# Kernel optimization log

Hardware: AMD Instinct MI355X
Metric: run time of the kernel (lower is better)

## Reference

```python
import jax, jax.numpy as jnp
import numpy as np
import math

VOCAB = 50257
BLOCK = 2048
NE = 768


def setup_inputs() -> dict:
    key = jax.random.key(0)
    ks = jax.random.split(key, 12)
    s = 0.02
    idx = jax.random.randint(ks[0], (4, 2048), 0, VOCAB, dtype=jnp.int64 if jax.config.jax_enable_x64 else jnp.int32)
    tok_emb = jax.random.normal(ks[1], (VOCAB, NE), jnp.float32) * s
    pos_emb = jax.random.normal(ks[2], (BLOCK, NE), jnp.float32) * s
    Wk = jax.random.normal(ks[3], (NE, NE), jnp.float32) * s
    bk = jnp.zeros((NE,), jnp.float32)
    Wq = jax.random.normal(ks[4], (NE, NE), jnp.float32) * s
    bq = jnp.zeros((NE,), jnp.float32)
    Wv = jax.random.normal(ks[5], (NE, NE), jnp.float32) * s
    bv = jnp.zeros((NE,), jnp.float32)
    ln_g = jnp.ones((NE,), jnp.float32)
    ln_b = jnp.zeros((NE,), jnp.float32)
    Wh = jax.random.normal(ks[6], (NE, VOCAB), jnp.float32) * s
    bh = jnp.zeros((VOCAB,), jnp.float32)
    return {"idx": idx, "tok_emb": tok_emb, "pos_emb": pos_emb, "Wq": Wq, "bq": bq,
            "Wk": Wk, "bk": bk, "Wv": Wv, "bv": bv, "ln_g": ln_g, "ln_b": ln_b,
            "Wh": Wh, "bh": bh}


def reference(idx, tok_emb, pos_emb, Wq, bq, Wk, bk, Wv, bv, ln_g, ln_b, Wh, bh):
    B, T = idx.shape
    C = tok_emb.shape[1]
    x = tok_emb[idx] + pos_emb[:T]  # [B,T,C]
    q = jnp.einsum('btc,cd->btd', x, Wq) + bq
    k = jnp.einsum('btc,cd->btd', x, Wk) + bk
    v = jnp.einsum('btc,cd->btd', x, Wv) + bv
    att = jnp.einsum('btd,bsd->bts', q, k) / math.sqrt(C)  # [B,T,T]
    causal = jnp.tril(jnp.ones((T, T), bool))
    att = jnp.where(causal, att, -jnp.inf)
    att = jax.nn.softmax(att, axis=-1)
    y = jnp.einsum('bts,bsd->btd', att, v)
    # LayerNorm (eps=1e-5, torch default)
    mu = jnp.mean(y, axis=-1, keepdims=True)
    var = jnp.mean((y - mu) ** 2, axis=-1, keepdims=True)
    yn = (y - mu) * jax.lax.rsqrt(var + 1e-5) * ln_g + ln_b
    logits = jnp.einsum('btc,cv->btv', yn, Wh) + bh
    return logits
```

## Files before the change

kernel.cpp:

```cpp
#include <hip/hip_runtime.h>
#include <hip/hip_bf16.h>
#include <math.h>

typedef __bf16 bf16x8 __attribute__((ext_vector_type(8)));
typedef float  f32x4  __attribute__((ext_vector_type(4)));

#define GAS(p) ((const __attribute__((address_space(1))) void*)(p))
#define LAS(p) ((__attribute__((address_space(3))) void*)(p))

static constexpr int NE = 768;

__global__ __launch_bounds__(256) void k_embed(const int* __restrict__ idx,
    const float* __restrict__ tok, const float* __restrict__ pos,
    __hip_bfloat16* __restrict__ xb)
{
    int bt = blockIdx.x;
    int t  = bt & 2047;
    int token = idx[bt];
    const float* te = tok + (size_t)token * NE;
    const float* pe = pos + (size_t)t * NE;
    __hip_bfloat16* o = xb + (size_t)bt * NE;
    for (int c = threadIdx.x; c < NE; c += 256)
        o[c] = __float2bfloat16(te[c] + pe[c]);
}

__global__ __launch_bounds__(256) void k_transpose_f32_bf16(
    const float* __restrict__ in, __hip_bfloat16* __restrict__ out,
    int R, int C, int outRows)
{
    __shared__ float tile[32][33];
    int c0 = blockIdx.x * 32, r0 = blockIdx.y * 32;
    int tx = threadIdx.x & 31, ty = threadIdx.x >> 5;
    #pragma unroll
    for (int i = 0; i < 32; i += 8) {
        int r = r0 + ty + i, c = c0 + tx;
        tile[ty + i][tx] = (r < R && c < C) ? in[(size_t)r * C + c] : 0.f;
    }
    __syncthreads();
    #pragma unroll
    for (int i = 0; i < 32; i += 8) {
        int oc = c0 + ty + i, orr = r0 + tx;
        if (oc < outRows && orr < R)
            out[(size_t)oc * R + orr] = __float2bfloat16(tile[tx][ty + i]);
    }
}

__global__ __launch_bounds__(256) void k_transpose_bf16(
    const __hip_bfloat16* __restrict__ in, __hip_bfloat16* __restrict__ out,
    int R, int C)
{
    __shared__ __hip_bfloat16 tile[32][33];
    size_t boff = (size_t)blockIdx.z * R * C;
    int c0 = blockIdx.x * 32, r0 = blockIdx.y * 32;
    int tx = threadIdx.x & 31, ty = threadIdx.x >> 5;
    #pragma unroll
    for (int i = 0; i < 32; i += 8)
        tile[ty + i][tx] = in[boff + (size_t)(r0 + ty + i) * C + (c0 + tx)];
    __syncthreads();
    #pragma unroll
    for (int i = 0; i < 32; i += 8)
        out[boff + (size_t)(c0 + ty + i) * R + (r0 + tx)] = tile[tx][ty + i];
}

__global__ __launch_bounds__(256) void k_pack_bias(const float* __restrict__ bq,
    const float* __restrict__ bk, const float* __restrict__ bv, float* __restrict__ o)
{
    int i = blockIdx.x * 256 + threadIdx.x;
    if (i < 768) o[i] = bq[i];
    else if (i < 1536) o[i] = bk[i - 768];
    else if (i < 2304) o[i] = bv[i - 1536];
}

template<int MODE>
__global__ __launch_bounds__(256) void k_gemm(
    const __hip_bfloat16* __restrict__ A, const __hip_bfloat16* __restrict__ Bt,
    int K, int lda, int ldb,
    size_t strideA, size_t strideB, size_t strideC,
    float* __restrict__ outf, int ldc, int ncols,
    const float* __restrict__ bias, float scale,
    __hip_bfloat16* __restrict__ oq, __hip_bfloat16* __restrict__ ok,
    __hip_bfloat16* __restrict__ ov)
{
    int bn = blockIdx.x, bm = blockIdx.y, bz = blockIdx.z;
    if constexpr (MODE == 2) bm = (int)gridDim.y - 1 - bm;
    if (MODE == 1 && bn > bm) return;
    __shared__ __align__(16) __hip_bfloat16 As[128 * 32];
    __shared__ __align__(16) __hip_bfloat16 Bs[128 * 32];
    const __hip_bfloat16* Ab = A  + bz * strideA + (size_t)bm * 128 * lda;
    const __hip_bfloat16* Bb = Bt + bz * strideB + (size_t)bn * 128 * ldb;
    int tid = threadIdx.x, w = tid >> 6, lane = tid & 63;
    int wr = w >> 1, wc = w & 1;
    f32x4 acc[4][4] = {};
    int sr = tid >> 2, sc = (tid & 3) * 8;
    int lr = lane & 15, lk = (lane >> 4) * 8;

    const int kend = (MODE == 2) ? (bm + 1) * 128 : K;

    for (int k0 = 0; k0 < kend; k0 += 32) {
        __syncthreads();
        #pragma unroll
        for (int i = 0; i < 2; ++i) {
            __builtin_amdgcn_global_load_lds(GAS(Ab + (size_t)(i * 64 + sr) * lda + k0 + sc),
                                             LAS((char*)As + i * 4096 + w * 1024), 16, 0, 0);
            __builtin_amdgcn_global_load_lds(GAS(Bb + (size_t)(i * 64 + sr) * ldb + k0 + sc),
                                             LAS((char*)Bs + i * 4096 + w * 1024), 16, 0, 0);
        }
        __syncthreads();
        bf16x8 af[4], bfv[4];
        #pragma unroll
        for (int mi = 0; mi < 4; ++mi)
            af[mi] = *(const bf16x8*)(As + (wr * 64 + mi * 16 + lr) * 32 + lk);
        #pragma unroll
        for (int ni = 0; ni < 4; ++ni)
            bfv[ni] = *(const bf16x8*)(Bs + (wc * 64 + ni * 16 + lr) * 32 + lk);
        #pragma unroll
        for (int mi = 0; mi < 4; ++mi)
            #pragma unroll
            for (int ni = 0; ni < 4; ++ni)
                acc[mi][ni] = __builtin_amdgcn_mfma_f32_16x16x32_bf16(af[mi], bfv[ni], acc[mi][ni], 0, 0, 0);
    }

    int r4 = (lane >> 4) * 4;
    #pragma unroll
    for (int mi = 0; mi < 4; ++mi) {
        #pragma unroll
        for (int ni = 0; ni < 4; ++ni) {
            #pragma unroll
            for (int r = 0; r < 4; ++r) {
                int row = bm * 128 + wr * 64 + mi * 16 + r4 + r;
                int col = bn * 128 + wc * 64 + ni * 16 + lr;
                float v = acc[mi][ni][r];
                if constexpr (MODE == 0) {
                    v += bias[col];
                    __hip_bfloat16 h = __float2bfloat16(v);
                    if (col < 768)       oq[(size_t)row * 768 + col]          = h;
                    else if (col < 1536) ok[(size_t)row * 768 + (col - 768)]  = h;
                    else                 ov[(size_t)row * 768 + (col - 1536)] = h;
                } else if constexpr (MODE == 1) {
                    outf[bz * strideC + (size_t)row * ldc + col] = v * scale;
                } else {
                    outf[bz * strideC + (size_t)row * ldc + col] = v;
                }
            }
        }
    }
}

__global__ __launch_bounds__(512, 2) void k_gemm_head(
    const __hip_bfloat16* __restrict__ A,
    const __hip_bfloat16* __restrict__ Bt,
    float* __restrict__ out, const float* __restrict__ bias, int ldc, int ncols)
{
    constexpr int K = 768, NT = K / 64, NI = NT / 2;
    __shared__ __align__(16) __hip_bfloat16 As[2][2][128 * 64];
    __shared__ __align__(16) __hip_bfloat16 Bs[2][2][128 * 64];

    const int Nx = (int)gridDim.x;
    const int qq = Nx >> 3, rr = Nx & 7;
    const int xcd = (int)blockIdx.x & 7, xidx = (int)blockIdx.x >> 3;
    const int bn = (xcd < rr ? xcd * (qq + 1) : rr * (qq + 1) + (xcd - rr) * qq) + xidx;
    const int bm = blockIdx.y;
    const int tid = threadIdx.x;
    const int w = tid >> 6, lane = tid & 63;
    const int wr = w >> 2, wc = w & 3;
    const int lr = lane & 15, lu = lane >> 4;

    const int sr = tid >> 3;
    const int su = (tid & 7) ^ (sr & 7);
    const __hip_bfloat16* Ap = A  + (size_t)(bm * 256) * K;
    const __hip_bfloat16* Bp = Bt + (size_t)(bn * 256) * K;

    f32x4 acc[8][4] = {};
    bf16x8 bq[4][2];

    auto stageAh = [&](int t, int h) {
        #pragma unroll
        for (int l = 0; l < 2; ++l)
            __builtin_amdgcn_global_load_lds(
                GAS(Ap + (size_t)(h * 128 + l * 64 + sr) * K + t * 64 + su * 8),
                LAS(&As[t & 1][h][l * 4096 + tid * 8]), 16, 0, 0);
    };
    auto stageBh = [&](int t, int h) {
        #pragma unroll
        for (int l = 0; l < 2; ++l)
            __builtin_amdgcn_global_load_lds(
                GAS(Bp + (size_t)(h * 128 + l * 64 + sr) * K + t * 64 + su * 8),
                LAS(&Bs[t & 1][h][l * 4096 + tid * 8]), 16, 0, 0);
    };
    auto rdA = [&](int b, int q, int f, int kk) {
        int row = q * 32 + f * 16 + lr;
        return *(const bf16x8*)&As[b][wr][row * 64 + (((kk * 4 + lu) ^ (row & 7)) << 3)];
    };
    auto rdB = [&](int b, int n, int kk) {
        int row = (wc & 1) * 64 + n * 16 + lr;
        return *(const bf16x8*)&Bs[b][wc >> 1][row * 64 + (((kk * 4 + lu) ^ (row & 7)) << 3)];
    };

#define BAR() asm volatile("s_barrier" ::: "memory")
#define VM4() asm volatile("s_waitcnt vmcnt(4)" ::: "memory")
#define VM0() asm volatile("s_waitcnt vmcnt(0)" ::: "memory")
#define CLUSTER(Q)                                                                                          \
    __builtin_amdgcn_s_setprio(1);                                                                          \
    _Pragma("unroll") for (int n = 0; n < 4; ++n)                                                           \
        acc[2*(Q)+0][n] = __builtin_amdgcn_mfma_f32_16x16x32_bf16(af[0][0], bq[n][0], acc[2*(Q)+0][n], 0, 0, 0); \
    _Pragma("unroll") for (int n = 0; n < 4; ++n)                                                           \
        acc[2*(Q)+1][n] = __builtin_amdgcn_mfma_f32_16x16x32_bf16(af[1][0], bq[n][0], acc[2*(Q)+1][n], 0, 0, 0); \
    _Pragma("unroll") for (int n = 0; n < 4; ++n)                                                           \
        acc[2*(Q)+0][n] = __builtin_amdgcn_mfma_f32_16x16x32_bf16(af[0][1], bq[n][1], acc[2*(Q)+0][n], 0, 0, 0); \
    _Pragma("unroll") for (int n = 0; n < 4; ++n)                                                           \
        acc[2*(Q)+1][n] = __builtin_amdgcn_mfma_f32_16x16x32_bf16(af[1][1], bq[n][1], acc[2*(Q)+1][n], 0, 0, 0); \
    __builtin_amdgcn_s_setprio(0);
#define PH(B_, Q_, STAGE)                                                       \
    {   bf16x8 af[2][2];                                                        \
        _Pragma("unroll") for (int f = 0; f < 2; ++f) {                         \
            af[f][0] = rdA(B_, Q_, f, 0); af[f][1] = rdA(B_, Q_, f, 1); }       \
        STAGE                                                                   \
        CLUSTER(Q_)                                                             \
        BAR(); }
#define PHV(B_, Q_, STAGE, VMSTMT)                                              \
    {   bf16x8 af[2][2];                                                        \
        _Pragma("unroll") for (int f = 0; f < 2; ++f) {                         \
            af[f][0] = rdA(B_, Q_, f, 0); af[f][1] = rdA(B_, Q_, f, 1); }       \
        STAGE                                                                   \
        VMSTMT                                                                  \
        BAR();                                                                  \
        CLUSTER(Q_)                                                             \
        BAR(); }

    stageBh(0, 0); stageBh(0, 1);
    stageAh(0, 0); stageAh(0, 1);
    stageBh(1, 0); stageBh(1, 1);
    VM4();
    BAR();

    for (int i = 0; i < NI; ++i) {
        const int t0 = 2 * i, t1 = 2 * i + 1;
        const bool full = (i + 1 < NI);
        #pragma unroll
        for (int n = 0; n < 4; ++n) { bq[n][0] = rdB(0, n, 0); bq[n][1] = rdB(0, n, 1); }
        PH(0, 0, { stageAh(t1, 0); stageAh(t1, 1); })
        PH(0, 1, { if (full) stageBh(t0 + 2, 0); })
        PH(0, 2, { if (full) stageBh(t0 + 2, 1); })
        PHV(0, 3, { }, { if (full) { VM4(); } else { VM0(); } })
        #pragma unroll
        for (int n = 0; n < 4; ++n) { bq[n][0] = rdB(1, n, 0); bq[n][1] = rdB(1, n, 1); }
        PH(1, 0, { if (full) stageAh(t0 + 2, 0); })
        PH(1, 1, { if (full) stageAh(t0 + 2, 1); })
        PH(1, 2, { if (full) stageBh(t1 + 2, 0); })
        PHV(1, 3, { if (full) stageBh(t1 + 2, 1); }, { if (full) { VM4(); } else { VM0(); } })
    }
#undef PHV
#undef PH
#undef CLUSTER
#undef VM0
#undef VM4
#undef BAR

    const int r4 = lu * 4;
    #pragma unroll
    for (int m = 0; m < 8; ++m) {
        #pragma unroll
        for (int n = 0; n < 4; ++n) {
            int col = bn * 256 + wc * 64 + n * 16 + lr;
            if (col < ncols) {
                float bv_ = bias[col];
                #pragma unroll
                for (int r = 0; r < 4; ++r) {
                    int row = bm * 256 + wr * 128 + m * 16 + r4 + r;
                    out[(size_t)row * ldc + col] = acc[m][n][r] + bv_;
                }
            }
        }
    }
}

__global__ __launch_bounds__(256) void k_softmax(const float* __restrict__ att,
    __hip_bfloat16* __restrict__ P, int T)
{
    int t = blockIdx.x, b = blockIdx.y;
    const float* row = att + ((size_t)b * T + t) * T;
    __hip_bfloat16* prow = P + ((size_t)b * T + t) * T;
    const int n = t + 1;
    const int nz = ((t >> 7) + 1) << 7;
    __shared__ float red[256];
    float4 v[2];
    float mx = -1e30f;
    #pragma unroll
    for (int j = 0; j < 2; ++j) {
        int e = (threadIdx.x + j * 256) * 4;
        v[j] = *(const float4*)(row + e);
        #pragma unroll
        for (int k = 0; k < 4; ++k)
            if (e + k < n) mx = fmaxf(mx, ((const float*)&v[j])[k]);
    }
    red[threadIdx.x] = mx; __syncthreads();
    for (int o = 128; o > 0; o >>= 1) {
        if (threadIdx.x < o) red[threadIdx.x] = fmaxf(red[threadIdx.x], red[threadIdx.x + o]);
        __syncthreads();
    }
    mx = red[0]; __syncthreads();
    float ev[8];
    float sum = 0.f;
    #pragma unroll
    for (int j = 0; j < 2; ++j) {
        int e = (threadIdx.x + j * 256) * 4;
        #pragma unroll
        for (int k = 0; k < 4; ++k) {
            float x = ((const float*)&v[j])[k];
            float ex = (e + k < n) ? __expf(x - mx) : 0.f;
            ev[j * 4 + k] = ex;
            sum += ex;
        }
    }
    red[threadIdx.x] = sum; __syncthreads();
    for (int o = 128; o > 0; o >>= 1) {
        if (threadIdx.x < o) red[threadIdx.x] += red[threadIdx.x + o];
        __syncthreads();
    }
    float inv = 1.f / red[0];
    #pragma unroll
    for (int j = 0; j < 2; ++j) {
        int e = (threadIdx.x + j * 256) * 4;
        #pragma unroll
        for (int k = 0; k < 4; ++k)
            if (e + k < nz) prow[e + k] = __float2bfloat16(ev[j * 4 + k] * inv);
    }
}

__global__ __launch_bounds__(256) void k_layernorm(const float* __restrict__ y,
    const float* __restrict__ g, const float* __restrict__ b,
    __hip_bfloat16* __restrict__ yn)
{
    int row = blockIdx.x;
    const float* yr = y + (size_t)row * NE;
    float s = 0.f, s2 = 0.f;
    for (int c = threadIdx.x; c < NE; c += 256) { float v = yr[c]; s += v; s2 += v * v; }
    __shared__ float r1[256], r2[256];
    r1[threadIdx.x] = s; r2[threadIdx.x] = s2; __syncthreads();
    for (int o = 128; o > 0; o >>= 1) {
        if (threadIdx.x < o) { r1[threadIdx.x] += r1[threadIdx.x + o]; r2[threadIdx.x] += r2[threadIdx.x + o]; }
        __syncthreads();
    }
    float mu = r1[0] / NE;
    float var = r2[0] / NE - mu * mu;
    float rs = rsqrtf(var + 1e-5f);
    __hip_bfloat16* o = yn + (size_t)row * NE;
    for (int c = threadIdx.x; c < NE; c += 256)
        o[c] = __float2bfloat16((yr[c] - mu) * rs * g[c] + b[c]);
}

extern "C" void kernel_launch(void* const* d_in, const int* in_sizes, int n_in,
                              void* d_out, int out_size, void* d_ws, size_t ws_size,
                              hipStream_t stream)
{
    const int*   idx  = (const int*)  d_in[0];
    const float* tok  = (const float*)d_in[1];
    const float* pos  = (const float*)d_in[2];
    const float* Wq   = (const float*)d_in[3];
    const float* bq   = (const float*)d_in[4];
    const float* Wk   = (const float*)d_in[5];
    const float* bk   = (const float*)d_in[6];
    const float* Wv   = (const float*)d_in[7];
    const float* bv   = (const float*)d_in[8];
    const float* ln_g = (const float*)d_in[9];
    const float* ln_b = (const float*)d_in[10];
    const float* Wh   = (const float*)d_in[11];
    const float* bh   = (const float*)d_in[12];
    float* out = (float*)d_out;

    const int B = 4, T = 2048, C = 768, V = 50257, Vp = 50432;

    char* p = (char*)d_ws;
    auto take = [&](size_t bytes) { char* r = p; p += (bytes + 255) & ~(size_t)255; return r; };
    __hip_bfloat16* xb    = (__hip_bfloat16*)take((size_t)B * T * C * 2);
    __hip_bfloat16* wqkvT = (__hip_bfloat16*)take((size_t)3 * C * C * 2);
    float*          bqkv  = (float*)take((size_t)3 * C * 4);
    __hip_bfloat16* qb    = (__hip_bfloat16*)take((size_t)B * T * C * 2);
    __hip_bfloat16* kb    = (__hip_bfloat16*)take((size_t)B * T * C * 2);
    __hip_bfloat16* vb    = (__hip_bfloat16*)take((size_t)B * T * C * 2);
    __hip_bfloat16* vT    = (__hip_bfloat16*)take((size_t)B * T * C * 2);
    float*          att   = (float*)take((size_t)B * T * T * 4);
    __hip_bfloat16* P     = (__hip_bfloat16*)take((size_t)B * T * T * 2);
    float*          y     = (float*)take((size_t)B * T * C * 4);
    __hip_bfloat16* yn    = (__hip_bfloat16*)take((size_t)B * T * C * 2);
    __hip_bfloat16* whT   = (__hip_bfloat16*)att;

    float scale = 1.0f / sqrtf((float)C);

    k_embed<<<dim3(B * T), 256, 0, stream>>>(idx, tok, pos, xb);
    k_transpose_f32_bf16<<<dim3(24, 24), 256, 0, stream>>>(Wq, wqkvT,             C, C, C);
    k_transpose_f32_bf16<<<dim3(24, 24), 256, 0, stream>>>(Wk, wqkvT + C * C,     C, C, C);
    k_transpose_f32_bf16<<<dim3(24, 24), 256, 0, stream>>>(Wv, wqkvT + 2 * C * C, C, C, C);
    k_pack_bias<<<dim3(9), 256, 0, stream>>>(bq, bk, bv, bqkv);

    k_gemm<0><<<dim3(18, 64, 1), 256, 0, stream>>>(xb, wqkvT, C, C, C, 0, 0, 0,
        nullptr, 0, 0, bqkv, 1.f, qb, kb, vb);

    k_transpose_bf16<<<dim3(24, 64, B), 256, 0, stream>>>(vb, vT, T, C);

    k_gemm<1><<<dim3(16, 16, B), 256, 0, stream>>>(qb, kb, C, C, C,
        (size_t)T * C, (size_t)T * C, (size_t)T * T, att, T, 0, nullptr, scale,
        nullptr, nullptr, nullptr);

    k_softmax<<<dim3(T, B), 256, 0, stream>>>(att, P, T);

    k_gemm<2><<<dim3(6, 16, B), 256, 0, stream>>>(P, vT, T, T, T,
        (size_t)T * T, (size_t)C * T, (size_t)T * C, y, C, 0, nullptr, 1.f,
        nullptr, nullptr, nullptr);

    k_transpose_f32_bf16<<<dim3(Vp / 32, 24), 256, 0, stream>>>(Wh, whT, C, V, Vp);

    k_layernorm<<<dim3(B * T), 256, 0, stream>>>(y, ln_g, ln_b, yn);

    k_gemm_head<<<dim3(Vp / 256, 32), 512, 0, stream>>>(yn, whT, out, bh, V, V);
}
```

Before: 1.213 ms.

## Route QKV and QK^T GEMMs through the pipelined 256x256 head kernel; vectorize Wh transpose

Generalizes the head GEMM into a templated 256x256-tile, 512-thread, double-buffered kernel and uses it for the QKV projection and the causal Q·K^T score GEMM, not only the head. The old 128x128 kernel is kept only for P·V. The Wh transpose now uses 64x64 tiles with float4 loads and bf16x8 stores to cut memory transaction overhead. Larger tiles launch fewer blocks (9x32 for QKV, 8x8x4 for scores), which may underfill the GPU, and the coarser tiles skip less of the causal triangle.

```diff
diff --git a/kernel.cpp b/kernel.cpp
--- a/kernel.cpp
+++ b/kernel.cpp
@@ -42,6 +42,46 @@
         int oc = c0 + ty + i, orr = r0 + tx;
         if (oc < outRows && orr < R)
             out[(size_t)oc * R + orr] = __float2bfloat16(tile[tx][ty + i]);
+    }
+}
+
+__global__ __launch_bounds__(256) void k_transpose_wh(
+    const float* __restrict__ in, __hip_bfloat16* __restrict__ out,
+    int R , int C )
+{
+    __shared__ float tile[64][65];
+    const int n0 = blockIdx.x * 64, k0 = blockIdx.y * 64;
+    const int t = threadIdx.x;
+    if (n0 + 64 <= C) {
+        #pragma unroll
+        for (int pass = 0; pass < 4; ++pass) {
+            int idx = pass * 256 + t;
+            int kr = idx >> 4, nc4 = (idx & 15) * 4;
+            float4 v = *(const float4*)(in + (size_t)(k0 + kr) * C + n0 + nc4);
+            tile[kr][nc4] = v.x; tile[kr][nc4 + 1] = v.y;
+            tile[kr][nc4 + 2] = v.z; tile[kr][nc4 + 3] = v.w;
+        }
+    } else {
+        #pragma unroll
+        for (int pass = 0; pass < 16; ++pass) {
+            int idx = pass * 256 + t;
+            int kr = idx >> 6, nc = idx & 63;
+            int c = n0 + nc;
+            tile[kr][nc] = (c < C) ? in[(size_t)(k0 + kr) * C + c] : 0.f;
+        }
+    }
+    __syncthreads();
+    #pragma unroll
+    for (int pass = 0; pass < 2; ++pass) {
+        int nr = pass * 32 + (t >> 3);
+        int kc = (t & 7) * 8;
+        bf16x8 v;
+        #pragma unroll
+        for (int j = 0; j < 8; ++j) {
+            __hip_bfloat16 h = __float2bfloat16(tile[kc + j][nr]);
+            v[j] = *reinterpret_cast<__bf16*>(&h);
+        }
+        *(bf16x8*)(out + (size_t)(n0 + nr) * R + k0 + kc) = v;
     }
 }
 
@@ -83,7 +123,6 @@
 {
     int bn = blockIdx.x, bm = blockIdx.y, bz = blockIdx.z;
     if constexpr (MODE == 2) bm = (int)gridDim.y - 1 - bm;
-    if (MODE == 1 && bn > bm) return;
     __shared__ __align__(16) __hip_bfloat16 As[128 * 32];
     __shared__ __align__(16) __hip_bfloat16 Bs[128 * 32];
     const __hip_bfloat16* Ab = A  + bz * strideA + (size_t)bm * 128 * lda;
@@ -129,27 +168,20 @@
             for (int r = 0; r < 4; ++r) {
                 int row = bm * 128 + wr * 64 + mi * 16 + r4 + r;
                 int col = bn * 128 + wc * 64 + ni * 16 + lr;
-                float v = acc[mi][ni][r];
-                if constexpr (MODE == 0) {
-                    v += bias[col];
-                    __hip_bfloat16 h = __float2bfloat16(v);
-                    if (col < 768)       oq[(size_t)row * 768 + col]          = h;
-                    else if (col < 1536) ok[(size_t)row * 768 + (col - 768)]  = h;
-                    else                 ov[(size_t)row * 768 + (col - 1536)] = h;
-                } else if constexpr (MODE == 1) {
-                    outf[bz * strideC + (size_t)row * ldc + col] = v * scale;
-                } else {
-                    outf[bz * strideC + (size_t)row * ldc + col] = v;
-                }
+                outf[bz * strideC + (size_t)row * ldc + col] = acc[mi][ni][r];
             }
         }
     }
 }
 
-__global__ __launch_bounds__(512, 2) void k_gemm_head(
-    const __hip_bfloat16* __restrict__ A,
-    const __hip_bfloat16* __restrict__ Bt,
-    float* __restrict__ out, const float* __restrict__ bias, int ldc, int ncols)
+template<int MODE>
+__global__ __launch_bounds__(512, 2) void k_gemm8(
+    const __hip_bfloat16* __restrict__ A, const __hip_bfloat16* __restrict__ Bt,
+    float* __restrict__ outf, int ldc, int ncols,
+    const float* __restrict__ bias, float scale,
+    __hip_bfloat16* __restrict__ oq, __hip_bfloat16* __restrict__ ok,
+    __hip_bfloat16* __restrict__ ov,
+    size_t strideA, size_t strideB, size_t strideC)
 {
     constexpr int K = 768, NT = K / 64, NI = NT / 2;
     __shared__ __align__(16) __hip_bfloat16 As[2][2][128 * 64];
@@ -159,7 +191,8 @@
     const int qq = Nx >> 3, rr = Nx & 7;
     const int xcd = (int)blockIdx.x & 7, xidx = (int)blockIdx.x >> 3;
     const int bn = (xcd < rr ? xcd * (qq + 1) : rr * (qq + 1) + (xcd - rr) * qq) + xidx;
-    const int bm = blockIdx.y;
+    const int bm = blockIdx.y, bz = blockIdx.z;
+    if (MODE == 1 && bn > bm) return;
     const int tid = threadIdx.x;
     const int w = tid >> 6, lane = tid & 63;
     const int wr = w >> 2, wc = w & 3;
@@ -167,8 +200,8 @@
 
     const int sr = tid >> 3;
     const int su = (tid & 7) ^ (sr & 7);
-    const __hip_bfloat16* Ap = A  + (size_t)(bm * 256) * K;
-    const __hip_bfloat16* Bp = Bt + (size_t)(bn * 256) * K;
+    const __hip_bfloat16* Ap = A  + bz * strideA + (size_t)(bm * 256) * K;
+    const __hip_bfloat16* Bp = Bt + bz * strideB + (size_t)(bn * 256) * K;
 
     f32x4 acc[8][4] = {};
     bf16x8 bq[4][2];
@@ -262,12 +295,30 @@
         #pragma unroll
         for (int n = 0; n < 4; ++n) {
             int col = bn * 256 + wc * 64 + n * 16 + lr;
-            if (col < ncols) {
+            if constexpr (MODE == 0) {
                 float bv_ = bias[col];
                 #pragma unroll
                 for (int r = 0; r < 4; ++r) {
                     int row = bm * 256 + wr * 128 + m * 16 + r4 + r;
-                    out[(size_t)row * ldc + col] = acc[m][n][r] + bv_;
+                    __hip_bfloat16 h = __float2bfloat16(acc[m][n][r] + bv_);
+                    if (col < 768)       oq[(size_t)row * 768 + col]          = h;
+                    else if (col < 1536) ok[(size_t)row * 768 + (col - 768)]  = h;
+                    else                 ov[(size_t)row * 768 + (col - 1536)] = h;
+                }
+            } else if constexpr (MODE == 1) {
+                #pragma unroll
+                for (int r = 0; r < 4; ++r) {
+                    int row = bm * 256 + wr * 128 + m * 16 + r4 + r;
+                    outf[bz * strideC + (size_t)row * ldc + col] = acc[m][n][r] * scale;
+                }
+            } else {
+                if (col < ncols) {
+                    float bv_ = bias[col];
+                    #pragma unroll
+                    for (int r = 0; r < 4; ++r) {
+                        int row = bm * 256 + wr * 128 + m * 16 + r4 + r;
+                        outf[(size_t)row * ldc + col] = acc[m][n][r] + bv_;
+                    }
                 }
             }
         }
@@ -393,14 +444,14 @@
     k_transpose_f32_bf16<<<dim3(24, 24), 256, 0, stream>>>(Wv, wqkvT + 2 * C * C, C, C, C);
     k_pack_bias<<<dim3(9), 256, 0, stream>>>(bq, bk, bv, bqkv);
 
-    k_gemm<0><<<dim3(18, 64, 1), 256, 0, stream>>>(xb, wqkvT, C, C, C, 0, 0, 0,
-        nullptr, 0, 0, bqkv, 1.f, qb, kb, vb);
+    k_gemm8<0><<<dim3(9, 32, 1), 512, 0, stream>>>(xb, wqkvT, nullptr, 0, 2304,
+        bqkv, 1.f, qb, kb, vb, 0, 0, 0);
 
     k_transpose_bf16<<<dim3(24, 64, B), 256, 0, stream>>>(vb, vT, T, C);
 
-    k_gemm<1><<<dim3(16, 16, B), 256, 0, stream>>>(qb, kb, C, C, C,
-        (size_t)T * C, (size_t)T * C, (size_t)T * T, att, T, 0, nullptr, scale,
-        nullptr, nullptr, nullptr);
+    k_gemm8<1><<<dim3(8, 8, B), 512, 0, stream>>>(qb, kb, att, T, T,
+        nullptr, scale, nullptr, nullptr, nullptr,
+        (size_t)T * C, (size_t)T * C, (size_t)T * T);
 
     k_softmax<<<dim3(T, B), 256, 0, stream>>>(att, P, T);
 
@@ -408,9 +459,10 @@
         (size_t)T * T, (size_t)C * T, (size_t)T * C, y, C, 0, nullptr, 1.f,
         nullptr, nullptr, nullptr);
 
-    k_transpose_f32_bf16<<<dim3(Vp / 32, 24), 256, 0, stream>>>(Wh, whT, C, V, Vp);
+    k_transpose_wh<<<dim3(Vp / 64, C / 64), 256, 0, stream>>>(Wh, whT, C, V);
 
     k_layernorm<<<dim3(B * T), 256, 0, stream>>>(y, ln_g, ln_b, yn);
 
-    k_gemm_head<<<dim3(Vp / 256, 32), 512, 0, stream>>>(yn, whT, out, bh, V, V);
-}
+    k_gemm8<3><<<dim3(Vp / 256, 32), 512, 0, stream>>>(yn, whT, out, V, V,
+        bh, 1.f, nullptr, nullptr, nullptr, 0, 0, 0);
+}
```

Result: faster. 1.189 ms (-2.0%).
